# Performance work log

Measured on AMD Instinct MI355X. Metric: run time of the kernel, lower is better.

## Reference

```python
import jax, jax.numpy as jnp
import numpy as np

H, ND, RD, VD = 16, 128, 64, 128  # heads, nope/rope/v head dims
EPS = 1e-6


def rmsnorm(x, g):
    return x * jax.lax.rsqrt(jnp.mean(x * x, axis=-1, keepdims=True) + EPS) * g


def apply_rope(x, cos, sin):
    # x: [B,T,h,D]; cos/sin: [1,T,1,D/2]; interleaved pair rotation
    x1, x2 = x[..., 0::2], x[..., 1::2]
    o1 = x1 * cos - x2 * sin
    o2 = x1 * sin + x2 * cos
    return jnp.stack([o1, o2], axis=-1).reshape(x.shape)


def setup_inputs() -> dict:
    key = jax.random.key(0)
    ks = jax.random.split(key, 10)
    B, T, D = 2, 2048, 2048
    QR, KVR = 1536, 512
    s = 0.02
    return {
        "x": jax.random.normal(ks[0], (B, T, D), jnp.float32),
        "w_cq": jax.random.normal(ks[1], (D, QR), jnp.float32) * s,
        "g_q": jnp.ones((QR,), jnp.float32),
        "w_ckv": jax.random.normal(ks[2], (D, KVR), jnp.float32) * s,
        "g_kv": jnp.ones((KVR,), jnp.float32),
        "w_dq_nope": jax.random.normal(ks[3], (QR, H * ND), jnp.float32) * s,
        "w_dq_rope": jax.random.normal(ks[4], (QR, H * RD), jnp.float32) * s,
        "w_dk_nope": jax.random.normal(ks[5], (KVR, H * ND), jnp.float32) * s,
        "w_dv": jax.random.normal(ks[6], (KVR, H * VD), jnp.float32) * s,
        "w_k_rope": jax.random.normal(ks[7], (D, RD), jnp.float32) * s,
        "w_out": jax.random.normal(ks[8], (H * VD, D), jnp.float32) * s,
    }


def reference(x, w_cq, g_q, w_ckv, g_kv, w_dq_nope, w_dq_rope,
              w_dk_nope, w_dv, w_k_rope, w_out):
    B, T, D = x.shape
    # low-rank latents + RMSNorm
    q_lat = rmsnorm(x @ w_cq, g_q)          # [B,T,QR]
    kv_lat = rmsnorm(x @ w_ckv, g_kv)        # [B,T,KVR]
    q_nope = (q_lat @ w_dq_nope).reshape(B, T, H, ND)
    q_rope = (q_lat @ w_dq_rope).reshape(B, T, H, RD)
    k_nope = (kv_lat @ w_dk_nope).reshape(B, T, H, ND)
    v = (kv_lat @ w_dv).reshape(B, T, H, VD)
    k_rope = (x @ w_k_rope).reshape(B, T, 1, RD)  # shared across heads
    # RoPE (start_pos = 0, no past_kv)
    pos = jnp.arange(T, dtype=jnp.float32)
    inv_freq = 1.0 / (10000.0 ** (jnp.arange(0, RD, 2, dtype=jnp.float32) / RD))
    ang = pos[:, None] * inv_freq[None, :]               # [T, RD/2]
    cos = jnp.cos(ang)[None, :, None, :]
    sin = jnp.sin(ang)[None, :, None, :]
    q_rope = apply_rope(q_rope, cos, sin)
    k_rope = apply_rope(k_rope, cos, sin)
    k_rope = jnp.broadcast_to(k_rope, (B, T, H, RD))
    q = jnp.concatenate([q_nope, q_rope], axis=-1).transpose(0, 2, 1, 3)  # [B,H,T,ND+RD]
    k = jnp.concatenate([k_nope, k_rope], axis=-1).transpose(0, 2, 1, 3)
    v_t = v.transpose(0, 2, 1, 3)                                        # [B,H,T,VD]
    # causal SDPA, scale = 1/sqrt(head_dim)
    scale = 1.0 / jnp.sqrt(jnp.asarray(ND + RD, jnp.float32))
    scores = jnp.einsum('bhqd,bhkd->bhqk', q, k) * scale
    causal = jnp.tril(jnp.ones((T, T), dtype=bool))
    scores = jnp.where(causal[None, None], scores, -jnp.inf)
    attn = jax.nn.softmax(scores, axis=-1)
    out = jnp.einsum('bhqk,bhkd->bhqd', attn, v_t)
    out = out.transpose(0, 2, 1, 3).reshape(B, T, H * VD) @ w_out        # [B,T,D]
    return out, k, v_t
```

## Files before the change

### kernel.cpp

```cpp
#include <hip/hip_runtime.h>
#include <cstdint>
#include <cstddef>

typedef _Float16 HT;
typedef _Float16 h8 __attribute__((ext_vector_type(8)));
typedef _Float16 h4 __attribute__((ext_vector_type(4)));
typedef float f32x4 __attribute__((ext_vector_type(4)));

constexpr int Tn  = 2048;
constexpr int Dm  = 2048;
constexpr int Hh  = 16;
constexpr int RDc = 64;
constexpr int QRc = 1536;
constexpr int KVRc= 512;
constexpr int BT  = 4096;

#define VWAIT(N) asm volatile("s_waitcnt vmcnt(" #N ")" ::: "memory")
#define SBAR()   __builtin_amdgcn_s_barrier()

__device__ __forceinline__ f32x4 mfma16(h8 a, h8 b, f32x4 c) {
    return __builtin_amdgcn_mfma_f32_16x16x32_f16(a, b, c, 0, 0, 0);
}
__device__ __forceinline__ void gload_lds16(const void* g, void* l) {
    __builtin_amdgcn_global_load_lds(
        (const __attribute__((address_space(1))) unsigned int*)g,
        (__attribute__((address_space(3))) unsigned int*)l, 16, 0, 0);
}

struct PrepArgs {
    const float* s[8];
    HT* d[8];
    int K[8], N[8], start[8];
    float2* cs;
    const float* x;
    HT* x16;
};

__global__ __launch_bounds__(256)
void prep_kernel(PrepArgs p)
{
    __shared__ float Ts[64][65];
    const int bid = blockIdx.x;
    const int tid = threadIdx.x;

    if (bid < 256) {
        const int idx = bid * 256 + tid;
        const int t = idx >> 5, i = idx & 31;
        const float ang = (float)t * exp2f(-(float)i * (13.287712379549449f / 32.f));
        p.cs[idx] = make_float2(cosf(ang), sinf(ang));
        return;
    }
    if (bid >= 4000) {
        const size_t i = ((size_t)(bid - 4000) * 256 + tid) * 8;
        f32x4 a = *reinterpret_cast<const f32x4*>(p.x + i);
        f32x4 b = *reinterpret_cast<const f32x4*>(p.x + i + 4);
        h8 v;
        #pragma unroll
        for (int j = 0; j < 4; j++) { v[j] = (HT)a[j]; v[4 + j] = (HT)b[j]; }
        *reinterpret_cast<h8*>(p.x16 + i) = v;
        return;
    }
    const int bx0 = bid - 256;
    int seg = 0;
    #pragma unroll
    for (int i = 1; i < 8; i++) if (bx0 >= p.start[i]) seg = i;
    const float* src = p.s[seg];
    HT* dst = p.d[seg];
    const int K = p.K[seg], N = p.N[seg];
    const int bx = bx0 - p.start[seg];
    const int nx = N >> 6;
    const int n0 = (bx % nx) * 64, k0 = (bx / nx) * 64;
    {
        const int r = tid >> 2, c0 = (tid & 3) * 16;
        const float* s = src + (size_t)(k0 + r) * N + n0 + c0;
        #pragma unroll
        for (int j = 0; j < 4; j++)
            *reinterpret_cast<f32x4*>(&Ts[r][c0 + j * 4]) = *reinterpret_cast<const f32x4*>(s + j * 4);
    }
    __syncthreads();
    {
        const int c = tid >> 2, kq = (tid & 3) * 16;
        h8 o0, o1;
        #pragma unroll
        for (int j = 0; j < 8; j++) { o0[j] = (HT)Ts[kq + j][c]; o1[j] = (HT)Ts[kq + 8 + j][c]; }
        HT* d = dst + (size_t)(n0 + c) * K + k0 + kq;
        *reinterpret_cast<h8*>(d)     = o0;
        *reinterpret_cast<h8*>(d + 8) = o1;
    }
}

template<int EPI>
__global__ __launch_bounds__(256)
void gemm16d(const HT* __restrict__ A, const HT* __restrict__ Bt, const int K,
             HT* __restrict__ o1, HT* __restrict__ o2, HT* __restrict__ o3,
             float* __restrict__ f1, float* __restrict__ f2,
             const float2* __restrict__ cstab)
{
    __shared__ HT As[2][4096];
    __shared__ HT Bs[2][4096];

    const int tid  = threadIdx.x;
    const int lane = tid & 63;
    const int l15  = lane & 15, l4 = lane >> 4;
    const int w    = tid >> 6;
    const int wr   = w >> 1, wc = w & 1;
    const int m0   = blockIdx.y * 128;
    const int n0   = blockIdx.x * 128;

    f32x4 acc[4][4] = {};
    const int nk = K >> 5;

    const int schunk = ((lane & 3) ^ ((lane >> 2) & 3) ^ ((lane >> 4) & 3)) * 8;

#define GSTAGE(as_, bs_, kt_) do {                                             \
    _Pragma("unroll")                                                          \
    for (int i_ = 0; i_ < 2; i_++) {                                           \
        const int row_ = (w * 2 + i_) * 16 + (lane >> 2);                      \
        gload_lds16(A  + (size_t)(m0 + row_) * K + (kt_) + schunk,             \
                    (as_) + (w * 2 + i_) * 512);                               \
        gload_lds16(Bt + (size_t)(n0 + row_) * K + (kt_) + schunk,             \
                    (bs_) + (w * 2 + i_) * 512);                               \
    } } while (0)

    GSTAGE(As[0], Bs[0], 0);

    const int sl = (l4 ^ (l15 & 3) ^ ((l15 >> 2) & 3)) * 8;

    for (int kt = 0; kt < nk; kt++) {
        HT* as = As[kt & 1];
        HT* bs = Bs[kt & 1];
        if (kt + 1 < nk) {
            GSTAGE(As[(kt + 1) & 1], Bs[(kt + 1) & 1], (kt + 1) * 32);
            VWAIT(4);
        } else {
            VWAIT(0);
        }
        SBAR();

        h8 af[4], bf[4];
        #pragma unroll
        for (int f = 0; f < 4; f++)
            af[f] = *reinterpret_cast<const h8*>(&as[(wr * 64 + f * 16 + l15) * 32 + sl]);
        #pragma unroll
        for (int g = 0; g < 4; g++)
            bf[g] = *reinterpret_cast<const h8*>(&bs[(wc * 64 + g * 16 + l15) * 32 + sl]);
        #pragma unroll
        for (int f = 0; f < 4; f++)
            #pragma unroll
            for (int g = 0; g < 4; g++)
                acc[f][g] = mfma16(af[f], bf[g], acc[f][g]);
        SBAR();
    }
#undef GSTAGE

    #pragma unroll
    for (int f = 0; f < 4; f++) {
        #pragma unroll
        for (int g = 0; g < 4; g++) {
            const int row = m0 + wr * 64 + f * 16 + l4 * 4;
            const int col = n0 + wc * 64 + g * 16 + l15;
            if constexpr (EPI == 3) {
                #pragma unroll
                for (int r = 0; r < 4; r++)
                    f1[(size_t)(row + r) * 2048 + col] = acc[f][g][r];
            } else if constexpr (EPI == 0) {
                if (col < 1536) {
                    #pragma unroll
                    for (int r = 0; r < 4; r++)
                        o1[(size_t)(row + r) * 1536 + col] = (HT)acc[f][g][r];
                } else if (col < 2048) {
                    #pragma unroll
                    for (int r = 0; r < 4; r++)
                        o2[(size_t)(row + r) * 512 + (col - 1536)] = (HT)acc[f][g][r];
                } else if (col < 2112) {
                    const int cc = col - 2048;
                    const int i = cc >> 1;
                    const bool odd = cc & 1;
                    #pragma unroll
                    for (int r = 0; r < 4; r++) {
                        const int t = (row + r) & (Tn - 1);
                        const float2 cs = cstab[t * 32 + i];
                        const float v = acc[f][g][r];
                        const float p = __shfl_xor(v, 1);
                        const float ov = odd ? p * cs.y + v * cs.x : v * cs.x - p * cs.y;
                        o3[(size_t)(row + r) * 64 + cc] = (HT)ov;
                    }
                }
            } else if constexpr (EPI == 1) {
                if (col < 2048) {
                    #pragma unroll
                    for (int r = 0; r < 4; r++)
                        o1[(size_t)(row + r) * 2048 + col] = (HT)acc[f][g][r];
                } else {
                    const int cc = col - 2048;
                    const int i = (cc & 63) >> 1;
                    const bool odd = cc & 1;
                    #pragma unroll
                    for (int r = 0; r < 4; r++) {
                        const int t = (row + r) & (Tn - 1);
                        const float2 cs = cstab[t * 32 + i];
                        const float v = acc[f][g][r];
                        const float p = __shfl_xor(v, 1);
                        const float ov = odd ? p * cs.y + v * cs.x : v * cs.x - p * cs.y;
                        o2[(size_t)(row + r) * 1024 + cc] = (HT)ov;
                    }
                }
            } else {
                if (col < 2048) {
                    const int h = col >> 7, d = col & 127;
                    #pragma unroll
                    for (int r = 0; r < 4; r++) {
                        const int rw = row + r;
                        const int b = rw >> 11, t = rw & (Tn - 1);
                        o1[(size_t)rw * 2048 + col] = (HT)acc[f][g][r];
                        f1[((size_t)(b * Hh + h) * Tn + t) * 192 + d] = acc[f][g][r];
                    }
                } else {
                    const int c2 = col - 2048;
                    const int h = c2 >> 7, d = c2 & 127;
                    const int b = row >> 11, t0 = row & (Tn - 1);
                    h4 pk;
                    #pragma unroll
                    for (int r = 0; r < 4; r++) {
                        f2[((size_t)(b * Hh + h) * Tn + t0 + r) * 128 + d] = acc[f][g][r];
                        pk[r] = (HT)acc[f][g][r];
                    }
                    *reinterpret_cast<h4*>(&o3[((size_t)(b * Hh + h) * 128 + d) * Tn + t0]) = pk;
                }
            }
        }
    }
}

__global__ __launch_bounds__(256)
void kropebc_kernel(const HT* __restrict__ kr16, float* __restrict__ out_k)
{
    const int idx = blockIdx.x * 256 + threadIdx.x;
    const int j4 = (idx & 15) * 4;
    const int t  = (idx >> 4) & (Tn - 1);
    const int b  = idx >> 15;
    h4 v = *reinterpret_cast<const h4*>(&kr16[((size_t)(b * Tn + t)) * 64 + j4]);
    f32x4 f;
    #pragma unroll
    for (int r = 0; r < 4; r++) f[r] = (float)v[r];
    #pragma unroll
    for (int h = 0; h < Hh; h++)
        *reinterpret_cast<f32x4*>(&out_k[((size_t)(b * Hh + h) * Tn + t) * 192 + 128 + j4]) = f;
}

__global__ __launch_bounds__(256)
void rmsnorm2_kernel(HT* __restrict__ Xa, const float* __restrict__ ga,
                     HT* __restrict__ Xb, const float* __restrict__ gb)
{
    const int which = blockIdx.y;
    HT* X = which ? Xb : Xa;
    const float* g = which ? gb : ga;
    const int N = which ? 512 : 1536;
    const int row = blockIdx.x;
    HT* x = X + (size_t)row * N;
    float ss = 0.f;
    for (int i = threadIdx.x * 8; i < N; i += 2048) {
        h8 v = *reinterpret_cast<const h8*>(&x[i]);
        #pragma unroll
        for (int j = 0; j < 8; j++) { float f = (float)v[j]; ss += f * f; }
    }
    #pragma unroll
    for (int sh = 32; sh >= 1; sh >>= 1) ss += __shfl_xor(ss, sh);
    __shared__ float red[4];
    if ((threadIdx.x & 63) == 0) red[threadIdx.x >> 6] = ss;
    __syncthreads();
    const float tot = red[0] + red[1] + red[2] + red[3];
    const float scale = rsqrtf(tot / (float)N + 1e-6f);
    for (int i = threadIdx.x * 8; i < N; i += 2048) {
        h8 v = *reinterpret_cast<const h8*>(&x[i]);
        f32x4 g0 = *reinterpret_cast<const f32x4*>(&g[i]);
        f32x4 g1 = *reinterpret_cast<const f32x4*>(&g[i + 4]);
        #pragma unroll
        for (int j = 0; j < 4; j++) { v[j]   = (HT)((float)v[j]   * scale * g0[j]);
                                      v[4+j] = (HT)((float)v[4+j] * scale * g1[j]); }
        *reinterpret_cast<h8*>(&x[i]) = v;
    }
}

__global__ __launch_bounds__(256, 2)
void attn10_kernel(const HT* __restrict__ qn, const HT* __restrict__ qr,
                   const HT* __restrict__ kn, const HT* __restrict__ kr16,
                   const HT* __restrict__ vt, HT* __restrict__ ao)
{
    __shared__ HT Ks_n[2][32 * 128];
    __shared__ HT Ks_r[2][32 * 64];
    __shared__ HT Vs[2][128 * 32];
    __shared__ HT Ps[4][32][40];

    const int tid  = threadIdx.x;
    const int lane = tid & 63;
    const int l15  = lane & 15, l4 = lane >> 4;
    const int w    = tid >> 6;

    const int bid = blockIdx.x;
    const int j   = bid >> 5;
    const int h   = bid & 15;
    const int b   = (bid >> 4) & 1;
    const int thi = 31 - j;

    const size_t bT = (size_t)b * Tn;
    const HT* vt_h = vt + ((size_t)(b * Hh + h) * 128) * Tn;

    const int qw0 = j   * 64 + w * 16;
    const int qw1 = thi * 64 + w * 16;

    h8 aq0[6], aq1[6];
    {
        const HT sc = (HT)(0.07216878364870323f * 1.4426950408889634f);
        const size_t rq0 = bT + qw0 + l15;
        const HT* pn = qn + rq0 * 2048 + h * 128 + l4 * 8;
        #pragma unroll
        for (int f = 0; f < 4; f++) aq0[f] = *reinterpret_cast<const h8*>(pn + f * 32) * sc;
        const HT* pr = qr + rq0 * 1024 + h * 64 + l4 * 8;
        aq0[4] = *reinterpret_cast<const h8*>(pr) * sc;
        aq0[5] = *reinterpret_cast<const h8*>(pr + 32) * sc;
        const size_t rq1 = bT + qw1 + l15;
        const HT* pn1 = qn + rq1 * 2048 + h * 128 + l4 * 8;
        #pragma unroll
        for (int f = 0; f < 4; f++) aq1[f] = *reinterpret_cast<const h8*>(pn1 + f * 32) * sc;
        const HT* pr1 = qr + rq1 * 1024 + h * 64 + l4 * 8;
        aq1[4] = *reinterpret_cast<const h8*>(pr1) * sc;
        aq1[5] = *reinterpret_cast<const h8*>(pr1 + 32) * sc;
    }

    f32x4 o0[8] = {}, o1[8] = {};
    float m0v[4] = {-1e30f, -1e30f, -1e30f, -1e30f};
    float m1v[4] = {-1e30f, -1e30f, -1e30f, -1e30f};
    float l0v[4] = {0.f, 0.f, 0.f, 0.f};
    float l1v[4] = {0.f, 0.f, 0.f, 0.f};

#define STAGE(sl_, kb_) do {                                                    \
    _Pragma("unroll")                                                           \
    for (int jj = 0; jj < 2; jj++) {                                            \
        const int cc = w * 2 + jj;                                              \
        const int r_ = cc * 4 + (lane >> 4);                                    \
        const int cl = (l15 & 8) | ((l15 & 7) ^ (r_ & 7));                      \
        gload_lds16(kn + (bT + (kb_) + r_) * 2048 + h * 128 + cl * 8,           \
                    &Ks_n[sl_][cc * 512]);                                      \
    }                                                                           \
    {                                                                           \
        const int r_ = w * 8 + (lane >> 3);                                     \
        const int cl = (lane & 7) ^ (r_ & 7);                                   \
        gload_lds16(kr16 + (bT + (kb_) + r_) * 64 + cl * 8,                     \
                    &Ks_r[sl_][w * 512]);                                       \
    }                                                                           \
    _Pragma("unroll")                                                           \
    for (int jj = 0; jj < 2; jj++) {                                            \
        const int cc = w * 2 + jj;                                              \
        const int d_ = cc * 16 + (lane >> 2);                                   \
        const int cl = (lane & 3) ^ ((d_ >> 1) & 3);                            \
        gload_lds16(vt_h + (size_t)d_ * Tn + (kb_) + cl * 8,                    \
                    &Vs[sl_][cc * 512]);                                        \
    } } while (0)

#define SMX(sv, mv, lv, ov, qwx, prow)                                          \
{                                                                               \
    float a_[4][2]; float mxr_[4]; bool ok_ = true;                             \
    _Pragma("unroll")                                                           \
    for (int r = 0; r < 4; r++) {                                               \
        const int qrow = (qwx) + l4 * 4 + r;                                    \
        _Pragma("unroll")                                                       \
        for (int c = 0; c < 2; c++)                                             \
            a_[r][c] = (kb + c * 16 + l15 <= qrow) ? sv[c][r] : -1e30f;         \
        mxr_[r] = fmaxf(a_[r][0], a_[r][1]);                                    \
        ok_ = ok_ && (mxr_[r] <= mv[r] + 8.f);                                  \
    }                                                                           \
    if (__builtin_expect((bool)__all(ok_), 1)) {                                \
        _Pragma("unroll")                                                       \
        for (int r = 0; r < 4; r++) {                                           \
            float rs = 0.f;                                                     \
            _Pragma("unroll")                                                   \
            for (int c = 0; c < 2; c++) {                                       \
                const float e = __builtin_exp2f(a_[r][c] - mv[r]);              \
                rs += e;                                                        \
                Ps[w][(prow) + l4 * 4 + r][c * 16 + l15] = (HT)e;               \
            }                                                                   \
            lv[r] += rs;                                                        \
        }                                                                       \
    } else {                                                                    \
        float al_[4];                                                           \
        _Pragma("unroll")                                                       \
        for (int r = 0; r < 4; r++) {                                           \
            float mx = mxr_[r];                                                 \
            _Pragma("unroll")                                                   \
            for (int sh = 1; sh < 16; sh <<= 1) mx = fmaxf(mx, __shfl_xor(mx, sh)); \
            const float mn = fmaxf(mv[r], mx);                                  \
            al_[r] = __builtin_exp2f(mv[r] - mn);                               \
            mv[r] = mn;                                                         \
            float rs = 0.f;                                                     \
            _Pragma("unroll")                                                   \
            for (int c = 0; c < 2; c++) {                                       \
                const float e = __builtin_exp2f(a_[r][c] - mn);                 \
                rs += e;                                                        \
                Ps[w][(prow) + l4 * 4 + r][c * 16 + l15] = (HT)e;               \
            }                                                                   \
            lv[r] = lv[r] * al_[r] + rs;                                        \
        }                                                                       \
        _Pragma("unroll")                                                       \
        for (int g = 0; g < 8; g++)                                             \
            _Pragma("unroll")                                                   \
            for (int r = 0; r < 4; r++) ov[g][r] *= al_[r];                     \
    }                                                                           \
}

#define KBODY(ACT0)                                                             \
{                                                                               \
    f32x4 s0[2] = {}, s1[2] = {};                                               \
    __builtin_amdgcn_s_setprio(1);                                              \
    _Pragma("unroll")                                                           \
    for (int c = 0; c < 2; c++) {                                               \
        const int kr = c * 16 + l15;                                            \
        const int sw = (kr & 7) << 4;                                           \
        const char* kbase = (const char*)&Ks_n[sl][0] + kr * 256;               \
        const char* rbase = (const char*)&Ks_r[sl][0] + kr * 128;               \
        const h8 br0 = *(const h8*)(rbase + ((l4 * 16) ^ sw));                  \
        const h8 br1 = *(const h8*)(rbase + ((64 + l4 * 16) ^ sw));             \
        _Pragma("unroll")                                                       \
        for (int f = 0; f < 4; f++) {                                           \
            const h8 kf = *(const h8*)(kbase + ((f * 64 + l4 * 16) ^ sw));      \
            s1[c] = mfma16(aq1[f], kf, s1[c]);                                  \
            if (ACT0) s0[c] = mfma16(aq0[f], kf, s0[c]);                        \
        }                                                                       \
        s1[c] = mfma16(aq1[4], br0, s1[c]);                                     \
        s1[c] = mfma16(aq1[5], br1, s1[c]);                                     \
        if (ACT0) { s0[c] = mfma16(aq0[4], br0, s0[c]);                         \
                    s0[c] = mfma16(aq0[5], br1, s0[c]); }                       \
    }                                                                           \
    __builtin_amdgcn_s_setprio(0);                                              \
    SMX(s1, m1v, l1v, o1, qw1, 16);                                             \
    if (ACT0) SMX(s0, m0v, l0v, o0, qw0, 0);                                    \
    const h8 ap1 = *reinterpret_cast<const h8*>(&Ps[w][16 + l15][l4 * 8]);      \
    h8 ap0 = ap1;                                                               \
    if (ACT0) ap0 = *reinterpret_cast<const h8*>(&Ps[w][l15][l4 * 8]);          \
    __builtin_amdgcn_s_setprio(1);                                              \
    _Pragma("unroll")                                                           \
    for (int g = 0; g < 8; g++) {                                               \
        const int d = g * 16 + l15;                                             \
        const int swd = ((d >> 1) & 3) << 4;                                    \
        const char* vbase = (const char*)&Vs[sl][0] + d * 64;                   \
        const h8 v0 = *(const h8*)(vbase + ((l4 * 16) ^ swd));                  \
        o1[g] = mfma16(ap1, v0, o1[g]);                                         \
        if (ACT0) o0[g] = mfma16(ap0, v0, o0[g]);                               \
    }                                                                           \
    __builtin_amdgcn_s_setprio(0);                                              \
}

    const int nkb = (thi + 1) * 2;
    STAGE(0, 0);

    for (int t = 0; t < nkb; t++) {
        const int kb = t * 32;
        const int sl = t & 1;
        if (t + 1 < nkb) {
            STAGE(sl ^ 1, kb + 32);
            VWAIT(5);
        } else {
            VWAIT(0);
        }
        SBAR();
        if (kb <= qw0 + 15)      KBODY(1)
        else if (kb <= qw1 + 15) KBODY(0)
        SBAR();
    }
#undef KBODY
#undef SMX
#undef STAGE

    {
        const size_t orow = bT + qw1 + l4 * 4;
        #pragma unroll
        for (int r = 0; r < 4; r++) {
            float rsum = l1v[r];
            #pragma unroll
            for (int sh = 1; sh < 16; sh <<= 1) rsum += __shfl_xor(rsum, sh);
            const float inv = 1.0f / rsum;
            HT* dst = ao + (orow + r) * 2048 + h * 128 + l15;
            #pragma unroll
            for (int g = 0; g < 8; g++) dst[g * 16] = (HT)(o1[g][r] * inv);
        }
    }
    {
        const size_t orow = bT + qw0 + l4 * 4;
        #pragma unroll
        for (int r = 0; r < 4; r++) {
            float rsum = l0v[r];
            #pragma unroll
            for (int sh = 1; sh < 16; sh <<= 1) rsum += __shfl_xor(rsum, sh);
            const float inv = 1.0f / rsum;
            HT* dst = ao + (orow + r) * 2048 + h * 128 + l15;
            #pragma unroll
            for (int g = 0; g < 8; g++) dst[g * 16] = (HT)(o0[g][r] * inv);
        }
    }
}

extern "C" void kernel_launch(void* const* d_in, const int* in_sizes, int n_in,
                              void* d_out, int out_size, void* d_ws, size_t ws_size,
                              hipStream_t stream)
{
    const float* x     = (const float*)d_in[0];
    const float* w_cq  = (const float*)d_in[1];
    const float* g_q   = (const float*)d_in[2];
    const float* w_ckv = (const float*)d_in[3];
    const float* g_kv  = (const float*)d_in[4];
    const float* w_dqn = (const float*)d_in[5];
    const float* w_dqr = (const float*)d_in[6];
    const float* w_dkn = (const float*)d_in[7];
    const float* w_dv  = (const float*)d_in[8];
    const float* w_kr  = (const float*)d_in[9];
    const float* w_out = (const float*)d_in[10];

    char* ws = (char*)d_ws;
    HT* cqT   = (HT*)(ws + 0);
    HT* ckvT  = (HT*)(ws + 6291456);
    HT* krT   = (HT*)(ws + 8388608);
    HT* dqnT  = (HT*)(ws + 8912896);
    HT* dqrT  = (HT*)(ws + 15204352);
    HT* dknT  = (HT*)(ws + 18350080);
    HT* dvT   = (HT*)(ws + 20447232);
    HT* outT  = (HT*)(ws + 22544384);
    HT* cq    = (HT*)(ws + 30932992);
    HT* ckv   = (HT*)(ws + 43515904);
    HT* qn    = (HT*)(ws + 47710208);
    HT* qr    = (HT*)(ws + 64487424);
    HT* kn    = (HT*)(ws + 72876032);
    HT* kr16  = (HT*)(ws + 89653248);
    HT* vt    = (HT*)(ws + 0);
    HT* x16   = qn;
    HT* ao    = qn;

    float* out_o = (float*)d_out;
    float* out_k = out_o + (size_t)BT * Dm;
    float* out_v = out_k + (size_t)2 * Hh * Tn * 192;
    float2* cstab = (float2*)out_v;

    const dim3 blk(256);

    PrepArgs pa;
    pa.s[0]=w_cq;  pa.d[0]=cqT;  pa.K[0]=2048; pa.N[0]=1536;
    pa.s[1]=w_ckv; pa.d[1]=ckvT; pa.K[1]=2048; pa.N[1]=512;
    pa.s[2]=w_kr;  pa.d[2]=krT;  pa.K[2]=2048; pa.N[2]=64;
    pa.s[3]=w_dqn; pa.d[3]=dqnT; pa.K[3]=1536; pa.N[3]=2048;
    pa.s[4]=w_dqr; pa.d[4]=dqrT; pa.K[4]=1536; pa.N[4]=1024;
    pa.s[5]=w_dkn; pa.d[5]=dknT; pa.K[5]=512;  pa.N[5]=2048;
    pa.s[6]=w_dv;  pa.d[6]=dvT;  pa.K[6]=512;  pa.N[6]=2048;
    pa.s[7]=w_out; pa.d[7]=outT; pa.K[7]=2048; pa.N[7]=2048;
    {
        int acc = 0;
        for (int i = 0; i < 8; i++) {
            pa.start[i] = acc;
            acc += (pa.N[i] >> 6) * (pa.K[i] >> 6);
        }
    }
    pa.cs = cstab; pa.x = x; pa.x16 = x16;
    prep_kernel<<<dim3(8096), blk, 0, stream>>>(pa);

    gemm16d<0><<<dim3(17, BT/128), blk, 0, stream>>>(x16, cqT, Dm,
        cq, ckv, kr16, nullptr, nullptr, cstab);
    kropebc_kernel<<<dim3(256), blk, 0, stream>>>(kr16, out_k);

    rmsnorm2_kernel<<<dim3(BT, 2), blk, 0, stream>>>(cq, g_q, ckv, g_kv);

    gemm16d<1><<<dim3(24, BT/128), blk, 0, stream>>>(cq, dqnT, QRc,
        qn, qr, nullptr, nullptr, nullptr, cstab);
    gemm16d<2><<<dim3(32, BT/128), blk, 0, stream>>>(ckv, dknT, KVRc,
        kn, nullptr, vt, out_k, out_v, nullptr);

    attn10_kernel<<<dim3(512), blk, 0, stream>>>(qn, qr, kn, kr16, vt, ao);

    gemm16d<3><<<dim3(16, BT/128), blk, 0, stream>>>(ao, outT, Dm,
        nullptr, nullptr, nullptr, out_o, nullptr, nullptr);
}
```

Baseline: 330.5 us.

## Split attention KV loop across two blocks with merge kernel; swizzle GEMM block order

The attention kernel now launches twice as many blocks. Each block processes alternating 32-key tiles (even or odd) and writes an unnormalised partial output plus per-row max and sum. A new merge kernel combines the two partials using log-sum-exp weights. Separately, the GEMM remaps linear block IDs into eight interleaved groups to change tile scheduling order across CUs/XCDs. The split is meant to raise occupancy and parallelism, at the cost of extra partial-output traffic, a fp16 intermediate and an additional launch.

```diff
diff --git a/kernel.cpp b/kernel.cpp
--- a/kernel.cpp
+++ b/kernel.cpp
@@ -104,8 +104,13 @@
     const int l15  = lane & 15, l4 = lane >> 4;
     const int w    = tid >> 6;
     const int wr   = w >> 1, wc = w & 1;
-    const int m0   = blockIdx.y * 128;
-    const int n0   = blockIdx.x * 128;
+
+    const int nxg = gridDim.x;
+    const int lin = blockIdx.y * nxg + blockIdx.x;
+    const int cpx = (nxg * gridDim.y) >> 3;
+    const int wg  = (lin & 7) * cpx + (lin >> 3);
+    const int m0  = (wg / nxg) * 128;
+    const int n0  = (wg % nxg) * 128;
 
     f32x4 acc[4][4] = {};
     const int nk = K >> 5;
@@ -283,9 +288,10 @@
 }
 
 __global__ __launch_bounds__(256, 2)
-void attn10_kernel(const HT* __restrict__ qn, const HT* __restrict__ qr,
+void attn11_kernel(const HT* __restrict__ qn, const HT* __restrict__ qr,
                    const HT* __restrict__ kn, const HT* __restrict__ kr16,
-                   const HT* __restrict__ vt, HT* __restrict__ ao)
+                   const HT* __restrict__ vt, HT* __restrict__ Op,
+                   float2* __restrict__ mlb)
 {
     __shared__ HT Ks_n[2][32 * 128];
     __shared__ HT Ks_r[2][32 * 64];
@@ -298,9 +304,11 @@
     const int w    = tid >> 6;
 
     const int bid = blockIdx.x;
-    const int j   = bid >> 5;
-    const int h   = bid & 15;
-    const int b   = (bid >> 4) & 1;
+    const int sp  = bid >> 9;
+    const int rst = bid & 511;
+    const int j   = rst >> 5;
+    const int h   = rst & 15;
+    const int b   = (rst >> 4) & 1;
     const int thi = 31 - j;
 
     const size_t bT = (size_t)b * Tn;
@@ -450,14 +458,14 @@
     __builtin_amdgcn_s_setprio(0);                                              \
 }
 
-    const int nkb = (thi + 1) * 2;
-    STAGE(0, 0);
-
-    for (int t = 0; t < nkb; t++) {
-        const int kb = t * 32;
+    const int cnt = thi + 1;
+    STAGE(0, sp * 32);
+
+    for (int t = 0; t < cnt; t++) {
+        const int kb = (2 * t + sp) * 32;
         const int sl = t & 1;
-        if (t + 1 < nkb) {
-            STAGE(sl ^ 1, kb + 32);
+        if (t + 1 < cnt) {
+            STAGE(sl ^ 1, kb + 64);
             VWAIT(5);
         } else {
             VWAIT(0);
@@ -471,32 +479,60 @@
 #undef SMX
 #undef STAGE
 
+    const size_t spO = (size_t)sp * BT * 2048;
     {
-        const size_t orow = bT + qw1 + l4 * 4;
         #pragma unroll
         for (int r = 0; r < 4; r++) {
             float rsum = l1v[r];
             #pragma unroll
             for (int sh = 1; sh < 16; sh <<= 1) rsum += __shfl_xor(rsum, sh);
-            const float inv = 1.0f / rsum;
-            HT* dst = ao + (orow + r) * 2048 + h * 128 + l15;
+            const float inv = rsum > 0.f ? 1.0f / rsum : 0.f;
+            const size_t row = bT + qw1 + l4 * 4 + r;
+            HT* dst = Op + spO + row * 2048 + h * 128 + l15;
             #pragma unroll
             for (int g = 0; g < 8; g++) dst[g * 16] = (HT)(o1[g][r] * inv);
+            if (l15 == 0)
+                mlb[(size_t)sp * (BT * 16) + row * 16 + h] = make_float2(m1v[r], rsum);
         }
     }
     {
-        const size_t orow = bT + qw0 + l4 * 4;
         #pragma unroll
         for (int r = 0; r < 4; r++) {
             float rsum = l0v[r];
             #pragma unroll
             for (int sh = 1; sh < 16; sh <<= 1) rsum += __shfl_xor(rsum, sh);
-            const float inv = 1.0f / rsum;
-            HT* dst = ao + (orow + r) * 2048 + h * 128 + l15;
+            const float inv = rsum > 0.f ? 1.0f / rsum : 0.f;
+            const size_t row = bT + qw0 + l4 * 4 + r;
+            HT* dst = Op + spO + row * 2048 + h * 128 + l15;
             #pragma unroll
             for (int g = 0; g < 8; g++) dst[g * 16] = (HT)(o0[g][r] * inv);
+            if (l15 == 0)
+                mlb[(size_t)sp * (BT * 16) + row * 16 + h] = make_float2(m0v[r], rsum);
         }
     }
+}
+
+__global__ __launch_bounds__(256)
+void attnmerge_kernel(const HT* __restrict__ Op, const float2* __restrict__ mlb,
+                      HT* __restrict__ ao)
+{
+    const size_t e = ((size_t)blockIdx.x * 256 + threadIdx.x) * 8;
+    const int row = (int)(e >> 11);
+    const int h   = (int)((e >> 7) & 15);
+    const float2 a = mlb[(size_t)row * 16 + h];
+    const float2 c = mlb[(size_t)BT * 16 + row * 16 + h];
+    const float m  = fmaxf(a.x, c.x);
+    const float c0 = a.y * exp2f(a.x - m);
+    const float c1 = c.y * exp2f(c.x - m);
+    const float inv = 1.0f / (c0 + c1);
+    const float w0 = c0 * inv, w1 = c1 * inv;
+    const h8 o0 = *reinterpret_cast<const h8*>(Op + e);
+    const h8 o1 = *reinterpret_cast<const h8*>(Op + (size_t)BT * 2048 + e);
+    h8 r;
+    #pragma unroll
+    for (int i = 0; i < 8; i++)
+        r[i] = (HT)((float)o0[i] * w0 + (float)o1[i] * w1);
+    *reinterpret_cast<h8*>(ao + e) = r;
 }
 
 extern "C" void kernel_launch(void* const* d_in, const int* in_sizes, int n_in,
@@ -533,11 +569,13 @@
     HT* vt    = (HT*)(ws + 0);
     HT* x16   = qn;
     HT* ao    = qn;
+    float2* mlb = (float2*)cq;
 
     float* out_o = (float*)d_out;
     float* out_k = out_o + (size_t)BT * Dm;
     float* out_v = out_k + (size_t)2 * Hh * Tn * 192;
     float2* cstab = (float2*)out_v;
+    HT* Opart = (HT*)out_o;
 
     const dim3 blk(256);
 
@@ -571,7 +609,9 @@
     gemm16d<2><<<dim3(32, BT/128), blk, 0, stream>>>(ckv, dknT, KVRc,
         kn, nullptr, vt, out_k, out_v, nullptr);
 
-    attn10_kernel<<<dim3(512), blk, 0, stream>>>(qn, qr, kn, kr16, vt, ao);
+    attn11_kernel<<<dim3(1024), blk, 0, stream>>>(qn, qr, kn, kr16, vt,
+        Opart, mlb);
+    attnmerge_kernel<<<dim3(4096), blk, 0, stream>>>(Opart, mlb, ao);
 
     gemm16d<3><<<dim3(16, BT/128), blk, 0, stream>>>(ao, outT, Dm,
         nullptr, nullptr, nullptr, out_o, nullptr, nullptr);
```

Result: no change. 337.0 us (+2.0%).
